# Optimization experiments

Hardware: AMD Instinct MI355X
Metric: run time of the kernel (lower is better)

The kernel has to match this reference:

```python
import jax, jax.numpy as jnp
import numpy as np


def _scan_dir(x, A, B, reverse):
    """First-order linear recurrence h_i = A*h_{i-1} + B*x_i along last axis (W).
    x: [Bsz, C, H, W]; A, B: [C]. reverse=True scans right-to-left but returns
    states in original index order (matching torch scan_backward)."""
    xs = jnp.moveaxis(x, -1, 0)  # [W, Bsz, C, H]
    Ab = A[None, :, None]
    Bb = B[None, :, None]
    def step(h, xi):
        h = Ab * h + Bb * xi
        return h, h
    h0 = jnp.zeros_like(xs[0])
    _, hs = jax.lax.scan(step, h0, xs, reverse=reverse)
    return jnp.moveaxis(hs, 0, -1)  # [Bsz, C, H, W]


def _conv1x1(x, W, b):
    # x: [B,Cin,H,W], W: [Cout,Cin], b: [Cout]
    return jnp.einsum('bchw,dc->bdhw', x, W) + b[None, :, None, None]


def setup_inputs() -> dict:
    key = jax.random.key(0)
    ks = jax.random.split(key, 10)
    B, C, H, W = 8, 64, 128, 128
    D = 128  # hidden_dim
    return {
        'F_in': jax.random.normal(ks[0], (B, C, H, W), dtype=jnp.float32),
        'prior': jax.random.uniform(ks[1], (B, 1, H, W), dtype=jnp.float32),
        'Wi': jax.random.normal(ks[2], (D, C), dtype=jnp.float32) * 0.05,
        'bi': jnp.zeros((D,), dtype=jnp.float32),
        'A_param': jax.random.normal(ks[3], (D,), dtype=jnp.float32),
        'B_param': jax.random.normal(ks[4], (D,), dtype=jnp.float32),
        'alpha': jnp.float32(0.1),
        'gamma': jnp.float32(0.1),
        'Wf': jax.random.normal(ks[5], (D, 4 * D), dtype=jnp.float32) * 0.05,
        'bf': jnp.zeros((D,), dtype=jnp.float32),
        'Wo': jax.random.normal(ks[6], (C, D), dtype=jnp.float32) * 0.05,
        'bo': jnp.zeros((C,), dtype=jnp.float32),
    }


def reference(F_in, prior, Wi, bi, A_param, B_param, alpha, gamma, Wf, bf, Wo, bo):
    # prior has 1 channel, repeated to C channels (prior already matches HxW)
    prior_r = jnp.broadcast_to(prior, F_in.shape)
    F_mod = F_in + alpha * prior_r
    x = _conv1x1(F_mod, Wi, bi)  # [B, D, H, W]
    A = jnp.tanh(A_param)
    Bp = B_param
    h_lr = _scan_dir(x, A, Bp, reverse=False)
    h_rl = _scan_dir(x, A, Bp, reverse=True)
    xt = jnp.swapaxes(x, 2, 3)  # scan over H axis
    h_tb = jnp.swapaxes(_scan_dir(xt, A, Bp, reverse=False), 2, 3)
    h_bt = jnp.swapaxes(_scan_dir(xt, A, Bp, reverse=True), 2, 3)
    h = jnp.concatenate([h_lr, h_rl, h_tb, h_bt], axis=1)  # [B, 4D, H, W]
    h = _conv1x1(h, Wf, bf)   # fusion -> [B, D, H, W]
    out = _conv1x1(h, Wo, bo)  # output_proj -> [B, C, H, W]
    return F_mod + gamma * out
```

## Files before the change

kernel.cpp:

```cpp
#include <hip/hip_runtime.h>
#include <hip/hip_bf16.h>

typedef unsigned int u32;
typedef unsigned short u16;
typedef float f32x2 __attribute__((ext_vector_type(2)));
typedef float f32x4 __attribute__((ext_vector_type(4)));
using bf16x8 = __attribute__((ext_vector_type(8))) short;
using f32x4v = __attribute__((ext_vector_type(4))) float;

#define DEVINL __device__ __forceinline__

constexpr int SCAN_LDS = 32768;
constexpr int XS = 132;
constexpr int LDS_X = 128 * XS * 2;

DEVINL float bf2f(u16 u) { union { u32 i; float f; } v; v.i = ((u32)u) << 16; return v.f; }
DEVINL float bf2f_lo(u32 u) { union { u32 i; float f; } v; v.i = u << 16; return v.f; }
DEVINL float bf2f_hi(u32 u) { union { u32 i; float f; } v; v.i = u & 0xffff0000u; return v.f; }
DEVINL u16 f2bf(float f) {
  __hip_bfloat16 h = __float2bfloat16(f);
  u16 r; __builtin_memcpy(&r, &h, 2); return r;
}
DEVINL u32 pack2(float a, float b) { return (u32)f2bf(a) | ((u32)f2bf(b) << 16); }

DEVINL void barrier_lgkm() {
  asm volatile("s_waitcnt lgkmcnt(0)" ::: "memory");
  __builtin_amdgcn_s_barrier();
  __builtin_amdgcn_sched_barrier(0);
}

__global__ __launch_bounds__(256) void k_pre(
    const float* __restrict__ Wf, const float* __restrict__ Wo,
    const float* __restrict__ bf_, const float* __restrict__ bo,
    const float* __restrict__ A_param, const float* __restrict__ Wi,
    float* __restrict__ A_t, float* __restrict__ beff,
    u16* __restrict__ Mrow, u16* __restrict__ Wi_bf) {
  const int wg = blockIdx.x, t = threadIdx.x;
  if (wg < 128) {
    const int idx = wg * 256 + t;
    const int cout = idx >> 9;
    const int k = idx & 511;
    float s = 0.f;
    for (int d = 0; d < 128; ++d) s = fmaf(Wo[cout * 128 + d], Wf[d * 512 + k], s);
    const int dir = k >> 7, dm = k & 127;
    Mrow[(dir * 64 + cout) * 128 + dm] = f2bf(s);
  } else if (wg == 128) {
    if (t < 128) A_t[t] = tanhf(A_param[t]);
    if (t < 64) {
      float s = bo[t];
      for (int d = 0; d < 128; ++d) s = fmaf(Wo[t * 128 + d], bf_[d], s);
      beff[t] = s;
    }
  } else {
#pragma unroll
    for (int k = 0; k < 32; ++k) {
      const int i = t + k * 256;
      Wi_bf[i] = f2bf(Wi[i]);
    }
  }
}

extern __shared__ char smem[];

template <bool REV>
DEVINL void scan_local(char* buf, int dp, int chunk, f32x2 A2) {
  f32x2 h = { 0.f, 0.f };
  const u32 cb = (u32)(dp * 4);
  const int s = chunk * 32;
  u32 nx[8];
#pragma unroll
  for (int j = 0; j < 8; ++j) {
    const int i = REV ? (127 - (s + j)) : (s + j);
    nx[j] = *(const u32*)(buf + i * 128 + (cb ^ ((u32)((i & 7) << 4))));
  }
  for (int ib = 0; ib < 32; ib += 8) {
    u32 cur[8];
#pragma unroll
    for (int j = 0; j < 8; ++j) cur[j] = nx[j];
    if (ib + 8 < 32) {
#pragma unroll
      for (int j = 0; j < 8; ++j) {
        const int i2 = s + ib + 8 + j;
        const int i = REV ? (127 - i2) : i2;
        nx[j] = *(const u32*)(buf + i * 128 + (cb ^ ((u32)((i & 7) << 4))));
      }
    }
#pragma unroll
    for (int j = 0; j < 8; ++j) {
      const int i2 = s + ib + j;
      const int i = REV ? (127 - i2) : i2;
      const f32x2 xv = { bf2f_lo(cur[j]), bf2f_hi(cur[j]) };
      h = A2 * h + xv;
      *(u32*)(buf + i * 128 + (cb ^ ((u32)((i & 7) << 4)))) = pack2(h.x, h.y);
    }
  }
}

template <bool REV>
DEVINL void scan_fix(char* buf, int dp, int chunk, f32x2 A2) {
  if (chunk == 0) return;
  f32x2 q = A2;
#pragma unroll
  for (int k = 0; k < 5; ++k) q *= q;
  const u32 cb = (u32)(dp * 4);
  f32x2 C = { 0.f, 0.f };
  for (int k = 0; k < chunk; ++k) {
    const int i2 = k * 32 + 31;
    const int i = REV ? (127 - i2) : i2;
    const u32 v = *(const u32*)(buf + i * 128 + (cb ^ ((u32)((i & 7) << 4))));
    const f32x2 xv = { bf2f_lo(v), bf2f_hi(v) };
    C = C * q + xv;
  }
  f32x2 p = A2;
  const int s = chunk * 32;
  u32 nx[8];
#pragma unroll
  for (int j = 0; j < 8; ++j) {
    const int i = REV ? (127 - (s + j)) : (s + j);
    nx[j] = *(const u32*)(buf + i * 128 + (cb ^ ((u32)((i & 7) << 4))));
  }
  for (int ib = 0; ib < 32; ib += 8) {
    u32 cur[8];
#pragma unroll
    for (int j = 0; j < 8; ++j) cur[j] = nx[j];
    if (ib + 8 < 32) {
#pragma unroll
      for (int j = 0; j < 8; ++j) {
        const int i2 = s + ib + 8 + j;
        const int i = REV ? (127 - i2) : i2;
        nx[j] = *(const u32*)(buf + i * 128 + (cb ^ ((u32)((i & 7) << 4))));
      }
    }
#pragma unroll
    for (int j = 0; j < 8; ++j) {
      const int i2 = s + ib + j;
      const int i = REV ? (127 - i2) : i2;
      const f32x2 xv = { bf2f_lo(cur[j]), bf2f_hi(cur[j]) };
      const f32x2 hv = p * C + xv;
      *(u32*)(buf + i * 128 + (cb ^ ((u32)((i & 7) << 4)))) = pack2(hv.x, hv.y);
      p *= A2;
    }
  }
}

DEVINL void run_scans(char* bufA, char* bufB, int t, int e, const float* __restrict__ A_t) {
  const int dp = t & 31, chunk = (t >> 5) & 3, dir = t >> 7;
  const f32x2 a = *(const f32x2*)(A_t + e * 64 + dp * 2);
  char* sb = dir ? bufB : bufA;
  if (dir == 0) scan_local<false>(sb, dp, chunk, a);
  else          scan_local<true >(sb, dp, chunk, a);
  __syncthreads();
  if (dir == 0) scan_fix<false>(sb, dp, chunk, a);
  else          scan_fix<true >(sb, dp, chunk, a);
}

DEVINL void combine64(const char* buf, const u16* __restrict__ Mrow, int dir, int e,
                      int lane, int wv, f32x4v (&acc2)[4][2]) {
  const int l15 = lane & 15, kg = lane >> 4;
#pragma unroll
  for (int ks = 0; ks < 2; ++ks) {
    bf16x8 afr[4], bfr[2];
#pragma unroll
    for (int ct = 0; ct < 4; ++ct)
      afr[ct] = *(const bf16x8*)(Mrow + ((size_t)dir * 64 + ct * 16 + l15) * 128 + e * 64 + ks * 32 + kg * 8);
#pragma unroll
    for (int pt = 0; pt < 2; ++pt) {
      const int row = wv * 32 + pt * 16 + l15;
      bfr[pt] = *(const bf16x8*)(buf + row * 128 + ((u32)(ks * 64 + kg * 16) ^ ((u32)((row & 7) << 4))));
    }
#pragma unroll
    for (int ct = 0; ct < 4; ++ct)
#pragma unroll
      for (int pt = 0; pt < 2; ++pt)
        acc2[ct][pt] = __builtin_amdgcn_mfma_f32_16x16x32_bf16(bfr[pt], afr[ct], acc2[ct][pt], 0, 0, 0);
  }
}

DEVINL void acc_to_outs(const f32x4v (&acc2)[4][2], int lane, int wv, char* buf) {
  const int l15 = lane & 15, kg = lane >> 4;
#pragma unroll
  for (int ct = 0; ct < 4; ++ct)
#pragma unroll
    for (int pt = 0; pt < 2; ++pt) {
      const int c = ct * 16 + l15;
      const int pos = wv * 32 + pt * 16 + kg * 4;
      *(f32x4v*)(buf + c * 512 + ((u32)(pos * 4) ^ ((u32)((c & 7) << 4)))) = acc2[ct][pt];
    }
}

DEVINL void outs_to_global(const char* buf, u16* __restrict__ og, int t) {
#pragma unroll
  for (int j = 0; j < 16; ++j) {
    const int i = t + j * 256;
    const int c = i >> 6, p2 = (i & 63) * 2;
    const f32x2 v = *(const f32x2*)(buf + c * 512 + ((u32)(p2 * 4) ^ ((u32)((c & 7) << 4))));
    *(u32*)(og + c * 128 + p2) = pack2(v.x, v.y);
  }
}

__global__ __launch_bounds__(256, 5) void k_A(
    const float* __restrict__ F_in, const float* __restrict__ prior,
    const u16* __restrict__ Wi_bf, const float* __restrict__ bi,
    const float* __restrict__ Bp, const float* __restrict__ alpha_p,
    const float* __restrict__ A_t, const u16* __restrict__ Mrow,
    u16* __restrict__ x2, u16* __restrict__ Shp) {
  char* bufA = smem;
  char* bufB = smem + 16384;

  const int t = threadIdx.x;
  const int lane = t & 63, wv = t >> 6, l15 = lane & 15, kg = lane >> 4;
  const int bid = blockIdx.x;
  const int b = bid >> 8, h = (bid >> 1) & 127, e = bid & 1;

  {
    const int w = t & 127, ch = t >> 7;
    const float alpha = alpha_p[0];
    const float pv = prior[(b * 128 + h) * 128 + w];
    const float* Fb = F_in + ((size_t)b * 64 + ch * 32) * 16384 + h * 128 + w;
    const u32 sw = (u32)((w & 7) << 4);
    char* rowp = bufA + w * 128;
#pragma unroll
    for (int q = 0; q < 4; ++q) {
      float fv[8];
#pragma unroll
      for (int j = 0; j < 8; ++j) fv[j] = fmaf(alpha, pv, Fb[(q * 8 + j) * 16384]);
      uint4 pk;
      pk.x = pack2(fv[0], fv[1]); pk.y = pack2(fv[2], fv[3]);
      pk.z = pack2(fv[4], fv[5]); pk.w = pack2(fv[6], fv[7]);
      *(uint4*)(rowp + ((u32)(ch * 64 + q * 16) ^ sw)) = pk;
    }
  }
  __syncthreads();

  bf16x8 bF[2][2];
#pragma unroll
  for (int wj = 0; wj < 2; ++wj)
#pragma unroll
    for (int ks = 0; ks < 2; ++ks) {
      const int row = wv * 32 + wj * 16 + l15;
      bF[wj][ks] = *(const bf16x8*)(bufA + row * 128 + ((u32)(ks * 64 + kg * 16) ^ ((u32)((row & 7) << 4))));
    }
  __syncthreads();

  {
    f32x4v acc[4][2];
#pragma unroll
    for (int dt = 0; dt < 4; ++dt) {
      const f32x4 bv = *(const f32x4*)(bi + e * 64 + dt * 16 + kg * 4);
      const f32x4v bvv = { bv.x, bv.y, bv.z, bv.w };
#pragma unroll
      for (int wj = 0; wj < 2; ++wj) acc[dt][wj] = bvv;
    }
#pragma unroll
    for (int ks = 0; ks < 2; ++ks)
#pragma unroll
      for (int dt = 0; dt < 4; ++dt) {
        const bf16x8 aWi = *(const bf16x8*)(Wi_bf + (e * 64 + dt * 16 + l15) * 64 + ks * 32 + kg * 8);
        acc[dt][0] = __builtin_amdgcn_mfma_f32_16x16x32_bf16(aWi, bF[0][ks], acc[dt][0], 0, 0, 0);
        acc[dt][1] = __builtin_amdgcn_mfma_f32_16x16x32_bf16(aWi, bF[1][ks], acc[dt][1], 0, 0, 0);
      }
#pragma unroll
    for (int dt = 0; dt < 4; ++dt) {
      const f32x4 B4 = *(const f32x4*)(Bp + e * 64 + dt * 16 + kg * 4);
      const f32x4v B4v = { B4.x, B4.y, B4.z, B4.w };
#pragma unroll
      for (int wj = 0; wj < 2; ++wj) {
        const f32x4v sv = acc[dt][wj] * B4v;
        const int w = wv * 32 + wj * 16 + l15;
        const int dl = dt * 16 + kg * 4;
        uint2 pk;
        pk.x = pack2(sv[0], sv[1]);
        pk.y = pack2(sv[2], sv[3]);
        const u32 col = (u32)(dl * 2) ^ ((u32)((w & 7) << 4));
        *(uint2*)(bufA + w * 128 + col) = pk;
        *(uint2*)(bufB + w * 128 + col) = pk;
      }
    }
  }
  barrier_lgkm();

  {
    u16* xg = x2 + (size_t)bid * 8192;
#pragma unroll
    for (int j = 0; j < 4; ++j) {
      const int idx = t + j * 256;
      const int row = idx >> 3, q = idx & 7;
      const uint4 v = *(const uint4*)(bufA + row * 128 + ((u32)(q * 16) ^ ((u32)((row & 7) << 4))));
      *(uint4*)(xg + row * 64 + q * 8) = v;
    }
  }
  barrier_lgkm();

  run_scans(bufA, bufB, t, e, A_t);
  __syncthreads();

  f32x4v acc2[4][2];
#pragma unroll
  for (int i = 0; i < 4; ++i)
#pragma unroll
    for (int j = 0; j < 2; ++j) acc2[i][j] = (f32x4v)0.f;
  combine64(bufA, Mrow, 0, e, lane, wv, acc2);
  combine64(bufB, Mrow, 1, e, lane, wv, acc2);
  __syncthreads();

  acc_to_outs(acc2, lane, wv, smem);
  __syncthreads();

  outs_to_global(smem, Shp + (size_t)bid * 8192, t);
}

__global__ __launch_bounds__(256, 5) void k_B(
    const u16* __restrict__ x2,
    const float* __restrict__ A_t, const u16* __restrict__ Mrow,
    u16* __restrict__ Svp) {
  char* bufA = smem;
  char* bufB = smem + 16384;
  const int t = threadIdx.x;
  const int lane = t & 63, wv = t >> 6;
  const int bid = blockIdx.x;
  const int b = bid >> 8, w = (bid >> 1) & 127, e = bid & 1;

#pragma unroll
  for (int j = 0; j < 4; ++j) {
    const int idx = t + j * 256;
    const int hh = idx >> 3, q = idx & 7;
    const uint4 v = *(const uint4*)(x2 + ((size_t)((b * 128 + hh) * 2 + e)) * 8192 + w * 64 + q * 8);
    const u32 col = (u32)(q * 16) ^ ((u32)((hh & 7) << 4));
    *(uint4*)(bufA + hh * 128 + col) = v;
    *(uint4*)(bufB + hh * 128 + col) = v;
  }
  __syncthreads();

  run_scans(bufA, bufB, t, e, A_t);
  __syncthreads();

  f32x4v acc2[4][2];
#pragma unroll
  for (int i = 0; i < 4; ++i)
#pragma unroll
    for (int j = 0; j < 2; ++j) acc2[i][j] = (f32x4v)0.f;
  combine64(bufA, Mrow, 2, e, lane, wv, acc2);
  combine64(bufB, Mrow, 3, e, lane, wv, acc2);
  __syncthreads();

  acc_to_outs(acc2, lane, wv, smem);
  __syncthreads();

  outs_to_global(smem, Svp + (size_t)bid * 8192, t);
}

__global__ __launch_bounds__(256) void k_final(
    const float* __restrict__ F_in, const float* __restrict__ prior,
    const float* __restrict__ alpha_p, const float* __restrict__ gamma_p,
    const float* __restrict__ beff, const u16* __restrict__ Svp,
    const u16* __restrict__ Shp, float* __restrict__ out) {
  u16* Xu = (u16*)smem;
  const int t = threadIdx.x;
  const int bid = blockIdx.x, b = bid >> 6, c = bid & 63;
  const size_t base = (size_t)bid * 16384;

  for (int i = t; i < 2048; i += 256) {
    const int w = i >> 4, q = i & 15;
    const u16* s0 = Svp + ((size_t)((b * 128 + w) * 2)) * 8192 + c * 128 + q * 8;
    const uint4 a4 = *(const uint4*)(s0);
    const uint4 b4 = *(const uint4*)(s0 + 8192);
    const u16* ap = (const u16*)&a4;
    const u16* bp = (const u16*)&b4;
    u32* dst = (u32*)(Xu + w * 132 + q * 8);
#pragma unroll
    for (int k = 0; k < 4; ++k) {
      const float lo = bf2f(ap[k * 2]) + bf2f(bp[k * 2]);
      const float hi = bf2f(ap[k * 2 + 1]) + bf2f(bp[k * 2 + 1]);
      dst[k] = pack2(lo, hi);
    }
  }
  __syncthreads();
  const float alpha = alpha_p[0], gamma = gamma_p[0];
  const float be = beff[c];
  for (int i = t; i < 2048; i += 256) {
    const int hh = i >> 4, w8 = (i & 15) * 8;
    const size_t off = base + hh * 128 + w8;
    const u16* sh0 = Shp + ((size_t)((b * 128 + hh) * 2)) * 8192 + c * 128 + w8;
    const uint4 g0 = *(const uint4*)(sh0);
    const uint4 g1 = *(const uint4*)(sh0 + 8192);
    const u16* p0 = (const u16*)&g0;
    const u16* p1 = (const u16*)&g1;
    const float* Fp = F_in + off;
    float* Op = out + off;
    const float* Pp = prior + (b * 128 + hh) * 128 + w8;
#pragma unroll
    for (int q = 0; q < 8; ++q) {
      const float sv = bf2f(Xu[(w8 + q) * 132 + hh]);
      Op[q] = Fp[q] + alpha * Pp[q] + gamma * (bf2f(p0[q]) + bf2f(p1[q]) + sv + be);
    }
  }
}

extern "C" void kernel_launch(void* const* d_in, const int* in_sizes, int n_in,
                              void* d_out, int out_size, void* d_ws, size_t ws_size,
                              hipStream_t stream) {
  const float* F_in   = (const float*)d_in[0];
  const float* prior  = (const float*)d_in[1];
  const float* Wi     = (const float*)d_in[2];
  const float* bi     = (const float*)d_in[3];
  const float* A_par  = (const float*)d_in[4];
  const float* B_par  = (const float*)d_in[5];
  const float* alpha  = (const float*)d_in[6];
  const float* gamma  = (const float*)d_in[7];
  const float* Wf     = (const float*)d_in[8];
  const float* bf_    = (const float*)d_in[9];
  const float* Wo     = (const float*)d_in[10];
  const float* bo     = (const float*)d_in[11];
  float* out = (float*)d_out;

  char* ws = (char*)d_ws;
  float* A_t   = (float*)ws;
  float* beff  = (float*)(ws + 512);
  u16*   Mrow  = (u16*)(ws + 1024);
  u16*   Wi_bf = (u16*)(ws + 66560);
  u16*   x2    = (u16*)(ws + 82944);
  u16*   Shp   = (u16*)(ws + 82944 + 33554432);
  u16*   Svp   = (u16*)(ws + 82944 + 67108864);

  hipFuncSetAttribute((const void*)k_A, hipFuncAttributeMaxDynamicSharedMemorySize, SCAN_LDS);
  hipFuncSetAttribute((const void*)k_B, hipFuncAttributeMaxDynamicSharedMemorySize, SCAN_LDS);

  k_pre  <<<130, 256, 0, stream>>>(Wf, Wo, bf_, bo, A_par, Wi, A_t, beff, Mrow, Wi_bf);
  k_A    <<<2048, 256, SCAN_LDS, stream>>>(F_in, prior, Wi_bf, bi, B_par, alpha, A_t, Mrow, x2, Shp);
  k_B    <<<2048, 256, SCAN_LDS, stream>>>(x2, A_t, Mrow, Svp);
  k_final<<<512, 256, LDS_X, stream>>>(F_in, prior, alpha, gamma, beff, Svp, Shp, out);
}
```

Measured before the change: 100.7 us.

## Process two tiles per block in k_A/k_B with register prefetch of next tile

k_A and k_B now launch half as many blocks, and each block handles two tiles (bid and bid+1024). The global loads for the second tile are issued into registers while the first tile is being computed, so load latency overlaps with compute. Several __syncthreads are also swapped for barrier_lgkm. The cost is higher register pressure from holding 32 extra floats (k_A) under launch bounds of 5 blocks, plus fewer blocks to spread across the CUs.

```diff
diff --git a/kernel.cpp b/kernel.cpp
--- a/kernel.cpp
+++ b/kernel.cpp
@@ -149,7 +149,7 @@
   char* sb = dir ? bufB : bufA;
   if (dir == 0) scan_local<false>(sb, dp, chunk, a);
   else          scan_local<true >(sb, dp, chunk, a);
-  __syncthreads();
+  barrier_lgkm();
   if (dir == 0) scan_fix<false>(sb, dp, chunk, a);
   else          scan_fix<true >(sb, dp, chunk, a);
 }
@@ -198,39 +198,42 @@
   }
 }
 
-__global__ __launch_bounds__(256, 5) void k_A(
-    const float* __restrict__ F_in, const float* __restrict__ prior,
-    const u16* __restrict__ Wi_bf, const float* __restrict__ bi,
-    const float* __restrict__ Bp, const float* __restrict__ alpha_p,
-    const float* __restrict__ A_t, const u16* __restrict__ Mrow,
-    u16* __restrict__ x2, u16* __restrict__ Shp) {
-  char* bufA = smem;
-  char* bufB = smem + 16384;
-
-  const int t = threadIdx.x;
-  const int lane = t & 63, wv = t >> 6, l15 = lane & 15, kg = lane >> 4;
-  const int bid = blockIdx.x;
-  const int b = bid >> 8, h = (bid >> 1) & 127, e = bid & 1;
-
-  {
-    const int w = t & 127, ch = t >> 7;
-    const float alpha = alpha_p[0];
-    const float pv = prior[(b * 128 + h) * 128 + w];
-    const float* Fb = F_in + ((size_t)b * 64 + ch * 32) * 16384 + h * 128 + w;
-    const u32 sw = (u32)((w & 7) << 4);
-    char* rowp = bufA + w * 128;
-#pragma unroll
-    for (int q = 0; q < 4; ++q) {
-      float fv[8];
-#pragma unroll
-      for (int j = 0; j < 8; ++j) fv[j] = fmaf(alpha, pv, Fb[(q * 8 + j) * 16384]);
-      uint4 pk;
-      pk.x = pack2(fv[0], fv[1]); pk.y = pack2(fv[2], fv[3]);
-      pk.z = pack2(fv[4], fv[5]); pk.w = pack2(fv[6], fv[7]);
-      *(uint4*)(rowp + ((u32)(ch * 64 + q * 16) ^ sw)) = pk;
-    }
-  }
-  __syncthreads();
+DEVINL void load_F(const float* __restrict__ F_in, const float* __restrict__ prior,
+                   float alpha, int b, int h, int t, float (&fv)[32]) {
+  const int w = t & 127, ch = t >> 7;
+  const float pv = prior[(b * 128 + h) * 128 + w];
+  const float* Fb = F_in + ((size_t)b * 64 + ch * 32) * 16384 + h * 128 + w;
+#pragma unroll
+  for (int q = 0; q < 4; ++q)
+#pragma unroll
+    for (int j = 0; j < 8; ++j)
+      fv[q * 8 + j] = fmaf(alpha, pv, Fb[(q * 8 + j) * 16384]);
+}
+
+DEVINL void stage_F(char* bufA, int t, const float (&fv)[32]) {
+  const int w = t & 127, ch = t >> 7;
+  const u32 sw = (u32)((w & 7) << 4);
+  char* rowp = bufA + w * 128;
+#pragma unroll
+  for (int q = 0; q < 4; ++q) {
+    uint4 pk;
+    pk.x = pack2(fv[q * 8 + 0], fv[q * 8 + 1]); pk.y = pack2(fv[q * 8 + 2], fv[q * 8 + 3]);
+    pk.z = pack2(fv[q * 8 + 4], fv[q * 8 + 5]); pk.w = pack2(fv[q * 8 + 6], fv[q * 8 + 7]);
+    *(uint4*)(rowp + ((u32)(ch * 64 + q * 16) ^ sw)) = pk;
+  }
+}
+
+template <bool PRE>
+DEVINL void tileA(char* bufA, char* bufB, int t, int lane, int wv, int l15, int kg,
+                  int tid, const float* __restrict__ F_in, const float* __restrict__ prior,
+                  float alpha, const u16* __restrict__ Wi_bf, const float* __restrict__ bi,
+                  const float* __restrict__ Bp, const float* __restrict__ A_t,
+                  const u16* __restrict__ Mrow, u16* __restrict__ x2, u16* __restrict__ Shp,
+                  const float (&fvcur)[32], float (&fvnext)[32], int tidnext) {
+  const int e = tid & 1;
+
+  stage_F(bufA, t, fvcur);
+  barrier_lgkm();
 
   bf16x8 bF[2][2];
 #pragma unroll
@@ -240,7 +243,7 @@
       const int row = wv * 32 + wj * 16 + l15;
       bF[wj][ks] = *(const bf16x8*)(bufA + row * 128 + ((u32)(ks * 64 + kg * 16) ^ ((u32)((row & 7) << 4))));
     }
-  __syncthreads();
+  barrier_lgkm();
 
   {
     f32x4v acc[4][2];
@@ -277,10 +280,12 @@
       }
     }
   }
+
+  if (PRE) load_F(F_in, prior, alpha, tidnext >> 8, (tidnext >> 1) & 127, t, fvnext);
   barrier_lgkm();
 
   {
-    u16* xg = x2 + (size_t)bid * 8192;
+    u16* xg = x2 + (size_t)tid * 8192;
 #pragma unroll
     for (int j = 0; j < 4; ++j) {
       const int idx = t + j * 256;
@@ -292,7 +297,7 @@
   barrier_lgkm();
 
   run_scans(bufA, bufB, t, e, A_t);
-  __syncthreads();
+  barrier_lgkm();
 
   f32x4v acc2[4][2];
 #pragma unroll
@@ -301,12 +306,80 @@
     for (int j = 0; j < 2; ++j) acc2[i][j] = (f32x4v)0.f;
   combine64(bufA, Mrow, 0, e, lane, wv, acc2);
   combine64(bufB, Mrow, 1, e, lane, wv, acc2);
-  __syncthreads();
-
-  acc_to_outs(acc2, lane, wv, smem);
-  __syncthreads();
-
-  outs_to_global(smem, Shp + (size_t)bid * 8192, t);
+  barrier_lgkm();
+
+  acc_to_outs(acc2, lane, wv, bufA);
+  barrier_lgkm();
+  outs_to_global(bufA, Shp + (size_t)tid * 8192, t);
+}
+
+__global__ __launch_bounds__(256, 5) void k_A(
+    const float* __restrict__ F_in, const float* __restrict__ prior,
+    const u16* __restrict__ Wi_bf, const float* __restrict__ bi,
+    const float* __restrict__ Bp, const float* __restrict__ alpha_p,
+    const float* __restrict__ A_t, const u16* __restrict__ Mrow,
+    u16* __restrict__ x2, u16* __restrict__ Shp) {
+  char* bufA = smem;
+  char* bufB = smem + 16384;
+  const int t = threadIdx.x;
+  const int lane = t & 63, wv = t >> 6, l15 = lane & 15, kg = lane >> 4;
+  const int bid = blockIdx.x;
+  const float alpha = alpha_p[0];
+
+  float fv0[32], fv1[32];
+  load_F(F_in, prior, alpha, bid >> 8, (bid >> 1) & 127, t, fv0);
+  tileA<true >(bufA, bufB, t, lane, wv, l15, kg, bid, F_in, prior, alpha,
+               Wi_bf, bi, Bp, A_t, Mrow, x2, Shp, fv0, fv1, bid + 1024);
+  barrier_lgkm();
+  tileA<false>(bufA, bufB, t, lane, wv, l15, kg, bid + 1024, F_in, prior, alpha,
+               Wi_bf, bi, Bp, A_t, Mrow, x2, Shp, fv1, fv1, 0);
+}
+
+DEVINL void load_X(const u16* __restrict__ x2, int b, int w, int e, int t, uint4 (&xv)[4]) {
+#pragma unroll
+  for (int j = 0; j < 4; ++j) {
+    const int idx = t + j * 256;
+    const int hh = idx >> 3, q = idx & 7;
+    xv[j] = *(const uint4*)(x2 + ((size_t)((b * 128 + hh) * 2 + e)) * 8192 + w * 64 + q * 8);
+  }
+}
+
+DEVINL void stage_X(char* bufA, char* bufB, int t, const uint4 (&xv)[4]) {
+#pragma unroll
+  for (int j = 0; j < 4; ++j) {
+    const int idx = t + j * 256;
+    const int hh = idx >> 3, q = idx & 7;
+    const u32 col = (u32)(q * 16) ^ ((u32)((hh & 7) << 4));
+    *(uint4*)(bufA + hh * 128 + col) = xv[j];
+    *(uint4*)(bufB + hh * 128 + col) = xv[j];
+  }
+}
+
+template <bool PRE>
+DEVINL void tileB(char* bufA, char* bufB, int t, int lane, int wv,
+                  int tid, const u16* __restrict__ x2, const float* __restrict__ A_t,
+                  const u16* __restrict__ Mrow, u16* __restrict__ Svp,
+                  const uint4 (&xcur)[4], uint4 (&xnext)[4], int tidnext) {
+  const int e = tid & 1;
+  stage_X(bufA, bufB, t, xcur);
+  if (PRE) load_X(x2, tidnext >> 8, (tidnext >> 1) & 127, tidnext & 1, t, xnext);
+  barrier_lgkm();
+
+  run_scans(bufA, bufB, t, e, A_t);
+  barrier_lgkm();
+
+  f32x4v acc2[4][2];
+#pragma unroll
+  for (int i = 0; i < 4; ++i)
+#pragma unroll
+    for (int j = 0; j < 2; ++j) acc2[i][j] = (f32x4v)0.f;
+  combine64(bufA, Mrow, 2, e, lane, wv, acc2);
+  combine64(bufB, Mrow, 3, e, lane, wv, acc2);
+  barrier_lgkm();
+
+  acc_to_outs(acc2, lane, wv, bufA);
+  barrier_lgkm();
+  outs_to_global(bufA, Svp + (size_t)tid * 8192, t);
 }
 
 __global__ __launch_bounds__(256, 5) void k_B(
@@ -318,35 +391,12 @@
   const int t = threadIdx.x;
   const int lane = t & 63, wv = t >> 6;
   const int bid = blockIdx.x;
-  const int b = bid >> 8, w = (bid >> 1) & 127, e = bid & 1;
-
-#pragma unroll
-  for (int j = 0; j < 4; ++j) {
-    const int idx = t + j * 256;
-    const int hh = idx >> 3, q = idx & 7;
-    const uint4 v = *(const uint4*)(x2 + ((size_t)((b * 128 + hh) * 2 + e)) * 8192 + w * 64 + q * 8);
-    const u32 col = (u32)(q * 16) ^ ((u32)((hh & 7) << 4));
-    *(uint4*)(bufA + hh * 128 + col) = v;
-    *(uint4*)(bufB + hh * 128 + col) = v;
-  }
-  __syncthreads();
-
-  run_scans(bufA, bufB, t, e, A_t);
-  __syncthreads();
-
-  f32x4v acc2[4][2];
-#pragma unroll
-  for (int i = 0; i < 4; ++i)
-#pragma unroll
-    for (int j = 0; j < 2; ++j) acc2[i][j] = (f32x4v)0.f;
-  combine64(bufA, Mrow, 2, e, lane, wv, acc2);
-  combine64(bufB, Mrow, 3, e, lane, wv, acc2);
-  __syncthreads();
-
-  acc_to_outs(acc2, lane, wv, smem);
-  __syncthreads();
-
-  outs_to_global(smem, Svp + (size_t)bid * 8192, t);
+
+  uint4 xv0[4], xv1[4];
+  load_X(x2, bid >> 8, (bid >> 1) & 127, bid & 1, t, xv0);
+  tileB<true >(bufA, bufB, t, lane, wv, bid, x2, A_t, Mrow, Svp, xv0, xv1, bid + 1024);
+  barrier_lgkm();
+  tileB<false>(bufA, bufB, t, lane, wv, bid + 1024, x2, A_t, Mrow, Svp, xv1, xv1, 0);
 }
 
 __global__ __launch_bounds__(256) void k_final(
@@ -426,7 +476,7 @@
   hipFuncSetAttribute((const void*)k_B, hipFuncAttributeMaxDynamicSharedMemorySize, SCAN_LDS);
 
   k_pre  <<<130, 256, 0, stream>>>(Wf, Wo, bf_, bo, A_par, Wi, A_t, beff, Mrow, Wi_bf);
-  k_A    <<<2048, 256, SCAN_LDS, stream>>>(F_in, prior, Wi_bf, bi, B_par, alpha, A_t, Mrow, x2, Shp);
-  k_B    <<<2048, 256, SCAN_LDS, stream>>>(x2, A_t, Mrow, Svp);
+  k_A    <<<1024, 256, SCAN_LDS, stream>>>(F_in, prior, Wi_bf, bi, B_par, alpha, A_t, Mrow, x2, Shp);
+  k_B    <<<1024, 256, SCAN_LDS, stream>>>(x2, A_t, Mrow, Svp);
   k_final<<<512, 256, LDS_X, stream>>>(F_in, prior, alpha, gamma, beff, Svp, Shp, out);
 }
```

Result: slower. 125.7 us (+24.9%).
